# Kernel optimization log

Hardware: AMD Instinct MI355X
Metric: run time of the kernel (lower is better)

The kernel has to match this reference:

```python
import jax, jax.numpy as jnp
import numpy as np

N, K, C, S = 40000, 16, 128, 8  # points, neighbors, channels, share_planes
EPS = 1e-5


def _bn(x, g, b, m, v):
    # eval-mode BatchNorm1d over the channel (last) axis
    return (x - m) * (g * jax.lax.rsqrt(v + EPS)) + b


def _forward(xyz, feats, Wq, bq, Wk, bk, Wv, bv, Wp1, bp1, p_gamma, p_beta, p_mean, p_var,
             Wp2, bp2, w_gamma, w_beta, w_mean, w_var, Ww1, bw1, w1_gamma, w1_beta,
             w1_mean, w1_var, Ww2, bw2, nei_ind):
    x = feats[0]          # (N, C)
    pos = xyz[0]          # (N, 3)
    idx = nei_ind[0]      # (N, K)

    q = x @ Wq + bq                      # (N, C)
    kf = (x @ Wk + bk)[idx]              # (N, K, C) neighbor gather
    vf = (x @ Wv + bv)[idx]              # (N, K, C)

    d = pos[idx] - pos[:, None, :]       # (N, K, 3) relative positions
    # linear_p: Linear_BN(3,3) -> ReLU -> Linear(3, C)
    p = jax.nn.relu(_bn(d @ Wp1 + bp1, p_gamma, p_beta, p_mean, p_var)) @ Wp2 + bp2  # (N, K, C)

    # mid_planes == out_planes, so the view(...,1,mid).sum(2) is an identity reshape
    w = kf - q[:, None, :] + p           # (N, K, C)
    w = _bn(w, w_gamma, w_beta, w_mean, w_var)  # bn_w over channels
    # linear_w: ReLU -> Linear_BN(C, C//S) -> ReLU -> Linear(C//S, C//S)
    w = jax.nn.relu(_bn(jax.nn.relu(w) @ Ww1 + bw1, w1_gamma, w1_beta, w1_mean, w1_var)) @ Ww2 + bw2  # (N, K, C//S)
    w = jax.nn.softmax(w, axis=1)        # softmax over K neighbors

    # grouped-channel weighted sum over neighbors
    agg = ((vf + p).reshape(N, K, S, C // S) * w[:, :, None, :]).sum(axis=1).reshape(N, C)

    # shortcut is Identity (in_planes == out_planes); broadcast over batch dim like torch
    return jax.nn.leaky_relu(agg[None, :, :] + feats, negative_slope=0.1)  # (1, N, C)


def setup_inputs() -> dict:
    key = jax.random.key(0)
    ks = jax.random.split(key, 16)
    f32 = jnp.float32

    def w(k, shape, scale):
        return jax.random.normal(k, shape, dtype=f32) * scale

    return {
        "xyz": jax.random.uniform(ks[0], (1, N, 3), dtype=f32),
        "feats": jax.random.normal(ks[1], (1, N, C), dtype=f32),
        "nei_ind": jax.random.randint(ks[2], (1, N, K), 0, N, dtype=jnp.int32),
        "Wq": w(ks[3], (C, C), C ** -0.5), "bq": jnp.zeros((C,), f32),
        "Wk": w(ks[4], (C, C), C ** -0.5), "bk": jnp.zeros((C,), f32),
        "Wv": w(ks[5], (C, C), C ** -0.5), "bv": jnp.zeros((C,), f32),
        "Wp1": w(ks[6], (3, 3), 0.5), "bp1": jnp.zeros((3,), f32),
        "p_gamma": jnp.ones((3,), f32), "p_beta": jnp.zeros((3,), f32),
        "p_mean": w(ks[7], (3,), 0.1), "p_var": jnp.ones((3,), f32),
        "Wp2": w(ks[8], (3, C), 0.5), "bp2": jnp.zeros((C,), f32),
        "w_gamma": jnp.ones((C,), f32), "w_beta": jnp.zeros((C,), f32),
        "w_mean": w(ks[9], (C,), 0.1), "w_var": jnp.ones((C,), f32),
        "Ww1": w(ks[10], (C, C // S), C ** -0.5), "bw1": jnp.zeros((C // S,), f32),
        "w1_gamma": jnp.ones((C // S,), f32), "w1_beta": jnp.zeros((C // S,), f32),
        "w1_mean": w(ks[11], (C // S,), 0.1), "w1_var": jnp.ones((C // S,), f32),
        "Ww2": w(ks[12], (C // S, C // S), (C // S) ** -0.5), "bw2": jnp.zeros((C // S,), f32),
    }


def reference(xyz, feats, nei_ind, Wq, bq, Wk, bk, Wv, bv, Wp1, bp1, p_gamma, p_beta,
              p_mean, p_var, Wp2, bp2, w_gamma, w_beta, w_mean, w_var, Ww1, bw1,
              w1_gamma, w1_beta, w1_mean, w1_var, Ww2, bw2):
    return _forward(xyz, feats, Wq, bq, Wk, bk, Wv, bv, Wp1, bp1, p_gamma, p_beta,
                    p_mean, p_var, Wp2, bp2, w_gamma, w_beta, w_mean, w_var, Ww1, bw1,
                    w1_gamma, w1_beta, w1_mean, w1_var, Ww2, bw2, nei_ind)
```

## Files before the change

kernel.cpp:

```cpp
#include <hip/hip_runtime.h>
#include <stdint.h>

#define N_PTS 40000
#define KNBR  16
#define CH    128
#define EPSV  1e-5f

typedef __attribute__((ext_vector_type(4))) float f32x4;
typedef __attribute__((ext_vector_type(2))) float f32x2;
typedef __attribute__((ext_vector_type(8))) short bf16x8;

__device__ __forceinline__ float bf2f(ushort u) {
    union { uint32_t i; float f; } x; x.i = ((uint32_t)u) << 16; return x.f;
}
__device__ __forceinline__ float bflo(uint32_t u) {
    union { uint32_t i; float f; } x; x.i = u << 16; return x.f;
}
__device__ __forceinline__ float bfhi(uint32_t u) {
    union { uint32_t i; float f; } x; x.i = u & 0xffff0000u; return x.f;
}
__device__ __forceinline__ ushort f2bf(float f) {
    union { float f; uint32_t i; } x; x.f = f;
    uint32_t i = x.i;
    i += 0x7fffu + ((i >> 16) & 1u);
    return (ushort)(i >> 16);
}
__device__ __forceinline__ f32x2 unpk2(uint32_t u) {
    f32x2 r; r.x = bflo(u); r.y = bfhi(u); return r;
}
__device__ __forceinline__ f32x2 vmax2(f32x2 a, f32x2 b) {
#if __has_builtin(__builtin_elementwise_max)
    return __builtin_elementwise_max(a, b);
#else
    f32x2 r; r.x = fmaxf(a.x, b.x); r.y = fmaxf(a.y, b.y); return r;
#endif
}

__device__ __forceinline__ float rfl(float x) {
    union { float f; int i; } u; u.f = x;
    u.i = __builtin_amdgcn_readfirstlane(u.i);
    return u.f;
}

#if __has_builtin(__builtin_amdgcn_cvt_pk_bf16_f32)
typedef __bf16 bf16x2v __attribute__((ext_vector_type(2)));
__device__ __forceinline__ uint32_t pack2(float a, float b) {
    union { bf16x2v v; uint32_t u; } x;
    x.v = __builtin_amdgcn_cvt_pk_bf16_f32(a, b);
    return x.u;
}
#else
__device__ __forceinline__ uint32_t pack2(float a, float b) {
    return (uint32_t)f2bf(a) | ((uint32_t)f2bf(b) << 16);
}
#endif

template <bool BF> struct IO;
template <> struct IO<true> {
    static __device__ __forceinline__ float  ld (const void* p, int i) { return bf2f(((const ushort*)p)[i]); }
    static __device__ __forceinline__ float2 ld2(const void* p, int i) { const uint32_t u = ((const uint32_t*)p)[i]; return make_float2(bflo(u), bfhi(u)); }
    static __device__ __forceinline__ ushort ldbf(const void* p, int i) { return ((const ushort*)p)[i]; }
    static __device__ __forceinline__ void   st2(void* p, int i, float a, float b) { ((uint32_t*)p)[i] = pack2(a, b); }
};
template <> struct IO<false> {
    static __device__ __forceinline__ float  ld (const void* p, int i) { return ((const float*)p)[i]; }
    static __device__ __forceinline__ float2 ld2(const void* p, int i) { return ((const float2*)p)[i]; }
    static __device__ __forceinline__ ushort ldbf(const void* p, int i) { return f2bf(((const float*)p)[i]); }
    static __device__ __forceinline__ void   st2(void* p, int i, float a, float b) { ((float2*)p)[i] = make_float2(a, b); }
};

__device__ __forceinline__ bool detect_bf16(const void* w_var) {
    return (*(const uint32_t*)w_var & 0xffffu) != 0u;
}

template <bool BF>
__device__ void wtrans_body(const void* Wq, const void* Wk, const void* Wv,
                            ushort* wt)
{
    const int m    = blockIdx.x >> 4;
    const int part = blockIdx.x & 15;
    const void* W = (m == 0) ? Wq : (m == 1) ? Wk : Wv;
    const int base = part * 1024 + threadIdx.x * 4;
    #pragma unroll
    for (int e = 0; e < 4; ++e) {
        const int idx = base + e;
        const int k = idx >> 7;
        const int c = idx & 127;
        wt[m * 16384 + c * 128 + k] = IO<BF>::ldbf(W, idx);
    }
}

__global__ __launch_bounds__(256) void wtrans_kernel(
    const void* Wq, const void* Wk, const void* Wv, const void* w_var_probe,
    ushort* wt)
{
    if (detect_bf16(w_var_probe)) wtrans_body<true >(Wq, Wk, Wv, wt);
    else                          wtrans_body<false>(Wq, Wk, Wv, wt);
}

#define PROJ_BLOCKS 1250
template <bool BF>
__device__ void proj_body(
    const void* feats, const ushort* __restrict__ wt,
    const void* bq, const void* bk, const void* bv,
    uint32_t* qws, uint4* kvws,
    ushort* xs, uint32_t* qs_s, uint32_t* kv_s)
{
    const int tid  = threadIdx.x;
    const int l    = tid & 63;
    const int w    = tid >> 6;
    const int t    = l & 15;
    const int quad = l >> 4;
    const int cq   = w;

    const void* bsrc[3] = { bq, bk, bv };

    bf16x8 afrag[3][4];
    float  bias[3][4];
    #pragma unroll
    for (int m = 0; m < 3; ++m) {
        const ushort* wtm = wt + m * 16384 + (cq * 16 + t) * 128 + quad * 8;
        #pragma unroll
        for (int s = 0; s < 4; ++s)
            afrag[m][s] = *(const bf16x8*)(wtm + s * 32);
        #pragma unroll
        for (int r = 0; r < 4; ++r)
            bias[m][r] = IO<BF>::ld(bsrc[m], cq * 16 + quad * 4 + r);
    }

    #pragma unroll 1
    for (int n = 0; n < 2; ++n) {
        const int tt = blockIdx.x + PROJ_BLOCKS * n;
        const int p0 = tt * 16;

        {
            const int r   = tid >> 5;
            const int c32 = tid & 31;
            if (BF) {
                const ushort4 v = *(const ushort4*)((const ushort*)feats + (p0 + r) * CH + c32 * 4);
                *(ushort4*)&xs[r * 136 + c32 * 4] = v;
            } else {
                const float4 v = *(const float4*)((const float*)feats + (p0 + r) * CH + c32 * 4);
                ushort4 o;
                o.x = f2bf(v.x); o.y = f2bf(v.y); o.z = f2bf(v.z); o.w = f2bf(v.w);
                *(ushort4*)&xs[r * 136 + c32 * 4] = o;
            }
        }
        __syncthreads();

        bf16x8 bfr[4];
        #pragma unroll
        for (int s = 0; s < 4; ++s)
            bfr[s] = *(const bf16x8*)&xs[t * 136 + quad * 8 + s * 32];

        f32x4 acc[3];
        #pragma unroll
        for (int m = 0; m < 3; ++m) {
            acc[m] = f32x4{ bias[m][0], bias[m][1], bias[m][2], bias[m][3] };
            #pragma unroll
            for (int s = 0; s < 4; ++s)
                acc[m] = __builtin_amdgcn_mfma_f32_16x16x32_bf16(afrag[m][s], bfr[s], acc[m], 0, 0, 0);
        }

        const int m16 = cq * 4 + quad;
        uint2 qo;
        qo.x = pack2(acc[0][0], acc[0][1]);
        qo.y = pack2(acc[0][2], acc[0][3]);
        *(uint2*)&qs_s[t * 66 + m16 * 2] = qo;
        uint4 kv;
        kv.x = pack2(acc[1][0], acc[1][1]);
        kv.y = pack2(acc[2][0], acc[2][1]);
        kv.z = pack2(acc[1][2], acc[1][3]);
        kv.w = pack2(acc[2][2], acc[2][3]);
        *(uint4*)&kv_s[t * 132 + m16 * 4] = kv;
        __syncthreads();

        {
            const int r = tid >> 5;
            const int u = tid & 31;
            ((uint2*)qws)[(p0 + r) * 32 + u] = *(const uint2*)&qs_s[r * 66 + u * 2];
            kvws[(p0 + r) * 32 + u]          = *(const uint4*)&kv_s[r * 132 + u * 4];
        }
    }
}

__global__ __launch_bounds__(512) void proj_kernel(
    const void* feats, const ushort* __restrict__ wt,
    const void* bq, const void* bk, const void* bv, const void* w_var_probe,
    uint32_t* qws, uint4* kvws)
{
    __shared__ ushort   xs[16 * 136];
    __shared__ uint32_t qs_s[16 * 66];
    __shared__ uint32_t kv_s[16 * 132];
    if (detect_bf16(w_var_probe))
        proj_body<true >(feats, wt, bq, bk, bv, qws, kvws, xs, qs_s, kv_s);
    else
        proj_body<false>(feats, wt, bq, bk, bv, qws, kvws, xs, qs_s, kv_s);
}

template <bool BF>
__device__ void attn_body(
    const void* xyz, const void* feats, const int* __restrict__ nei,
    const uint32_t* __restrict__ qws, const uint2* __restrict__ kvws,
    const void* Wp1, const void* bp1, const void* p_gamma, const void* p_beta,
    const void* p_mean, const void* p_var, const void* Wp2, const void* bp2,
    const void* w_gamma, const void* w_beta, const void* w_mean, const void* w_var,
    const void* Ww1, const void* bw1, const void* w1_gamma, const void* w1_beta,
    const void* w1_mean, const void* w1_var, const void* Ww2, const void* bw2,
    void* out, ushort* wbuf, ushort* ubuf, float* wsm, float* hlds,
    int i0, int l)
{
    const int t = l & 15;
    const int quad = l >> 4;

    float A1[3][3], C1[3];
    #pragma unroll
    for (int b = 0; b < 3; ++b) {
        const float sb = IO<BF>::ld(p_gamma, b) * rsqrtf(IO<BF>::ld(p_var, b) + EPSV);
        C1[b] = rfl((IO<BF>::ld(bp1, b) - IO<BF>::ld(p_mean, b)) * sb + IO<BF>::ld(p_beta, b));
        #pragma unroll
        for (int a = 0; a < 3; ++a) A1[a][b] = rfl(IO<BF>::ld(Wp1, a * 3 + b) * sb);
    }

    const float2 vg = IO<BF>::ld2(w_gamma, l);
    const float2 vb = IO<BF>::ld2(w_beta, l);
    const float2 vm = IO<BF>::ld2(w_mean, l);
    const float2 vv = IO<BF>::ld2(w_var, l);
    f32x2 scwv, shwv;
    scwv.x = vg.x * rsqrtf(vv.x + EPSV);
    scwv.y = vg.y * rsqrtf(vv.y + EPSV);
    shwv.x = vb.x - vm.x * scwv.x;
    shwv.y = vb.y - vm.y * scwv.y;

    f32x2 wp2v[3];
    #pragma unroll
    for (int r = 0; r < 3; ++r) {
        const float2 u = IO<BF>::ld2(Wp2, r * 64 + l);
        wp2v[r].x = u.x; wp2v[r].y = u.y;
    }
    const float2 vbp2 = IO<BF>::ld2(bp2, l);
    f32x2 bp2v; bp2v.x = vbp2.x; bp2v.y = vbp2.y;

    bf16x8 bfrag1[4];
    #pragma unroll
    for (int s = 0; s < 4; ++s)
        #pragma unroll
        for (int kk = 0; kk < 8; ++kk) {
            const int k = s * 32 + quad * 8 + kk;
            bfrag1[s][kk] = (short)IO<BF>::ldbf(Ww1, k * 16 + t);
        }
    bf16x8 bfrag2;
    #pragma unroll
    for (int kk = 0; kk < 8; ++kk) {
        const int k = quad * 8 + kk;
        bfrag2[kk] = (quad < 2) ? (short)IO<BF>::ldbf(Ww2, k * 16 + t) : (short)0;
    }

    const float s1t  = IO<BF>::ld(w1_gamma, t) * rsqrtf(IO<BF>::ld(w1_var, t) + EPSV);
    const float sh1t = IO<BF>::ld(w1_beta, t) - IO<BF>::ld(w1_mean, t) * s1t;
    const float bw1t = IO<BF>::ld(bw1, t);
    const float bw2t = IO<BF>::ld(bw2, t);

    #pragma unroll 1
    for (int pp = 0; pp < 4; ++pp) {
        const int i = i0 + pp;

        const uint32_t uq = qws[i * 64 + l];
        const f32x2 qsv = shwv - unpk2(uq) * scwv;

        const float pix = IO<BF>::ld(xyz, i * 3 + 0);
        const float piy = IO<BF>::ld(xyz, i * 3 + 1);
        const float piz = IO<BF>::ld(xyz, i * 3 + 2);

        const int vnj = nei[i * KNBR + t];
        const float ndx = IO<BF>::ld(xyz, vnj * 3 + 0) - pix;
        const float ndy = IO<BF>::ld(xyz, vnj * 3 + 1) - piy;
        const float ndz = IO<BF>::ld(xyz, vnj * 3 + 2) - piz;
        const float hh0 = fmaxf(0.f, ndx * A1[0][0] + ndy * A1[1][0] + ndz * A1[2][0] + C1[0]);
        const float hh1 = fmaxf(0.f, ndx * A1[0][1] + ndy * A1[1][1] + ndz * A1[2][1] + C1[1]);
        const float hh2 = fmaxf(0.f, ndx * A1[0][2] + ndy * A1[1][2] + ndz * A1[2][2] + C1[2]);
        if (quad == 0)
            *(float4*)&hlds[t * 4] = make_float4(hh0, hh1, hh2, 0.f);

        int njs[KNBR];
        #pragma unroll
        for (int j = 0; j < KNBR; ++j) njs[j] = nei[i * KNBR + j];
        uint2 kv[KNBR];
        #pragma unroll
        for (int j = 0; j < KNBR; ++j) kv[j] = kvws[njs[j] * 64 + l];

        uint32_t vpk[KNBR];
        #pragma unroll
        for (int j = 0; j < KNBR; ++j) {
            const float4 h = *(const float4*)&hlds[j * 4];
            const f32x2 pv = h.x * wp2v[0] + h.y * wp2v[1] + h.z * wp2v[2] + bp2v;
            vpk[j] = kv[j].y;
            const f32x2 wv = vmax2((unpk2(kv[j].x) + pv) * scwv + qsv,
                                   f32x2{0.f, 0.f});
            ((uint32_t*)wbuf)[j * 68 + l] = pack2(wv.x, wv.y);
        }

        f32x4 acc1 = { bw1t, bw1t, bw1t, bw1t };
        const ushort* arow = &wbuf[t * 136 + quad * 8];
        #pragma unroll
        for (int s = 0; s < 4; ++s) {
            const bf16x8 afrag = *(const bf16x8*)(arow + s * 32);
            acc1 = __builtin_amdgcn_mfma_f32_16x16x32_bf16(afrag, bfrag1[s], acc1, 0, 0, 0);
        }
        #pragma unroll
        for (int r = 0; r < 4; ++r) {
            const float u = fmaxf(0.f, acc1[r] * s1t + sh1t);
            ubuf[(quad * 4 + r) * 24 + t] = f2bf(u);
        }

        f32x4 acc2 = { bw2t, bw2t, bw2t, bw2t };
        bf16x8 afrag2;
        if (quad < 2) {
            afrag2 = *(const bf16x8*)(&ubuf[t * 24 + quad * 8]);
        } else {
            #pragma unroll
            for (int kk = 0; kk < 8; ++kk) afrag2[kk] = 0;
        }
        acc2 = __builtin_amdgcn_mfma_f32_16x16x32_bf16(afrag2, bfrag2, acc2, 0, 0, 0);

        float z0 = acc2[0], z1 = acc2[1], z2 = acc2[2], z3 = acc2[3];
        float mx = fmaxf(fmaxf(z0, z1), fmaxf(z2, z3));
        mx = fmaxf(mx, __shfl_xor(mx, 16));
        mx = fmaxf(mx, __shfl_xor(mx, 32));
        const float e0 = __expf(z0 - mx), e1 = __expf(z1 - mx);
        const float e2 = __expf(z2 - mx), e3 = __expf(z3 - mx);
        float ssum = e0 + e1 + e2 + e3;
        ssum += __shfl_xor(ssum, 16);
        ssum += __shfl_xor(ssum, 32);
        const float inv = 1.0f / ssum;
        wsm[(quad * 4 + 0) * 17 + t] = e0 * inv;
        wsm[(quad * 4 + 1) * 17 + t] = e1 * inv;
        wsm[(quad * 4 + 2) * 17 + t] = e2 * inv;
        wsm[(quad * 4 + 3) * 17 + t] = e3 * inv;

        const int t0 = (2 * l) & 15;
        f32x2 aggv = { 0.f, 0.f };
        #pragma unroll
        for (int j = 0; j < KNBR; ++j) {
            f32x2 wp;
            wp.x = wsm[j * 17 + t0];
            wp.y = wsm[j * 17 + t0 + 1];
            const float4 h = *(const float4*)&hlds[j * 4];
            const f32x2 pv = h.x * wp2v[0] + h.y * wp2v[1] + h.z * wp2v[2] + bp2v;
            aggv += (unpk2(vpk[j]) + pv) * wp;
        }
        const float2 xf = IO<BF>::ld2(feats, i * 64 + l);
        f32x2 ov; ov.x = aggv.x + xf.x; ov.y = aggv.y + xf.y;
        ov = vmax2(ov, 0.1f * ov);
        IO<BF>::st2(out, i * 64 + l, ov.x, ov.y);
    }
}

__global__ __launch_bounds__(256) void attn_kernel(
    const void* xyz, const void* feats, const int* __restrict__ nei,
    const uint32_t* __restrict__ qws, const uint2* __restrict__ kvws,
    const void* Wp1, const void* bp1, const void* p_gamma, const void* p_beta,
    const void* p_mean, const void* p_var, const void* Wp2, const void* bp2,
    const void* w_gamma, const void* w_beta, const void* w_mean, const void* w_var,
    const void* Ww1, const void* bw1, const void* w1_gamma, const void* w1_beta,
    const void* w1_mean, const void* w1_var, const void* Ww2, const void* bw2,
    void* out)
{
    __shared__ ushort wbuf[4][16 * 136];
    __shared__ float  hlds[4][16 * 4];

    const int wave = threadIdx.x >> 6;
    const int l    = threadIdx.x & 63;
    const int i0   = blockIdx.x * 16 + wave * 4;

    ushort* wb  = wbuf[wave];
    ushort* ub  = wb;
    float*  wsm = (float*)((char*)wb + 1024);

    if (detect_bf16(w_var))
        attn_body<true >(xyz, feats, nei, qws, kvws, Wp1, bp1, p_gamma, p_beta,
                         p_mean, p_var, Wp2, bp2, w_gamma, w_beta, w_mean, w_var,
                         Ww1, bw1, w1_gamma, w1_beta, w1_mean, w1_var, Ww2, bw2,
                         out, wb, ub, wsm, hlds[wave], i0, l);
    else
        attn_body<false>(xyz, feats, nei, qws, kvws, Wp1, bp1, p_gamma, p_beta,
                         p_mean, p_var, Wp2, bp2, w_gamma, w_beta, w_mean, w_var,
                         Ww1, bw1, w1_gamma, w1_beta, w1_mean, w1_var, Ww2, bw2,
                         out, wb, ub, wsm, hlds[wave], i0, l);
}

extern "C" void kernel_launch(void* const* d_in, const int* in_sizes, int n_in,
                              void* d_out, int out_size, void* d_ws, size_t ws_size,
                              hipStream_t stream) {
    const void* xyz     = d_in[0];
    const void* feats   = d_in[1];
    const int*  nei     = (const int*)d_in[2];
    const void* Wq      = d_in[3];
    const void* bq      = d_in[4];
    const void* Wk      = d_in[5];
    const void* bk      = d_in[6];
    const void* Wv      = d_in[7];
    const void* bv      = d_in[8];
    const void* Wp1     = d_in[9];
    const void* bp1     = d_in[10];
    const void* p_gamma = d_in[11];
    const void* p_beta  = d_in[12];
    const void* p_mean  = d_in[13];
    const void* p_var   = d_in[14];
    const void* Wp2     = d_in[15];
    const void* bp2     = d_in[16];
    const void* w_gamma = d_in[17];
    const void* w_beta  = d_in[18];
    const void* w_mean  = d_in[19];
    const void* w_var   = d_in[20];
    const void* Ww1     = d_in[21];
    const void* bw1     = d_in[22];
    const void* w1_gamma= d_in[23];
    const void* w1_beta = d_in[24];
    const void* w1_mean = d_in[25];
    const void* w1_var  = d_in[26];
    const void* Ww2     = d_in[27];
    const void* bw2     = d_in[28];

    uint32_t* qws  = (uint32_t*)d_ws;
    uint4*    kvws = (uint4*)(qws + (size_t)N_PTS * 64);

    const size_t base = (size_t)N_PTS * 64 * 4 + (size_t)N_PTS * 32 * 16;
    ushort* wt = (ws_size >= base + 3 * 16384 * sizeof(ushort))
               ? (ushort*)((char*)d_ws + base)
               : (ushort*)d_out;

    wtrans_kernel<<<48, 256, 0, stream>>>(Wq, Wk, Wv, w_var, wt);
    proj_kernel<<<PROJ_BLOCKS, 512, 0, stream>>>(feats, wt, bq, bk, bv, w_var,
                                                 qws, kvws);
    attn_kernel<<<N_PTS / 16, 256, 0, stream>>>(xyz, feats, nei, qws, (const uint2*)kvws,
                                          Wp1, bp1, p_gamma, p_beta, p_mean, p_var,
                                          Wp2, bp2, w_gamma, w_beta, w_mean, w_var,
                                          Ww1, bw1, w1_gamma, w1_beta, w1_mean, w1_var,
                                          Ww2, bw2, d_out);
}
```

Measured before the change: 214.9 us.

## Process more points per wave, cache v+p in registers, separate LDS buffers

Doubles the points handled per wave, so each block covers 32 points and the per-wave setup of weight fragments and BN constants is amortised over more points, at the cost of half as many blocks. The v+p values are now computed once in the first neighbor loop and kept as float pairs in registers, replacing the recomputation of the position encoding in the aggregation loop but raising register pressure. The ubuf and wsm scratch arrays get their own LDS regions instead of aliasing wbuf, the softmax weights use stride 18 so they can be read as 8-byte vectors, and the readfirstlane hints on the scalar constants are dropped.

```diff
diff --git a/kernel.cpp b/kernel.cpp
--- a/kernel.cpp
+++ b/kernel.cpp
@@ -5,6 +5,9 @@
 #define KNBR  16
 #define CH    128
 #define EPSV  1e-5f
+
+#define PTS_PER_WAVE 8
+#define PTS_PER_BLOCK (PTS_PER_WAVE * 4)
 
 typedef __attribute__((ext_vector_type(4))) float f32x4;
 typedef __attribute__((ext_vector_type(2))) float f32x2;
@@ -34,12 +37,6 @@
 #else
     f32x2 r; r.x = fmaxf(a.x, b.x); r.y = fmaxf(a.y, b.y); return r;
 #endif
-}
-
-__device__ __forceinline__ float rfl(float x) {
-    union { float f; int i; } u; u.f = x;
-    u.i = __builtin_amdgcn_readfirstlane(u.i);
-    return u.f;
 }
 
 #if __has_builtin(__builtin_amdgcn_cvt_pk_bf16_f32)
@@ -217,9 +214,9 @@
     #pragma unroll
     for (int b = 0; b < 3; ++b) {
         const float sb = IO<BF>::ld(p_gamma, b) * rsqrtf(IO<BF>::ld(p_var, b) + EPSV);
-        C1[b] = rfl((IO<BF>::ld(bp1, b) - IO<BF>::ld(p_mean, b)) * sb + IO<BF>::ld(p_beta, b));
-        #pragma unroll
-        for (int a = 0; a < 3; ++a) A1[a][b] = rfl(IO<BF>::ld(Wp1, a * 3 + b) * sb);
+        C1[b] = (IO<BF>::ld(bp1, b) - IO<BF>::ld(p_mean, b)) * sb + IO<BF>::ld(p_beta, b);
+        #pragma unroll
+        for (int a = 0; a < 3; ++a) A1[a][b] = IO<BF>::ld(Wp1, a * 3 + b) * sb;
     }
 
     const float2 vg = IO<BF>::ld2(w_gamma, l);
@@ -262,7 +259,7 @@
     const float bw2t = IO<BF>::ld(bw2, t);
 
     #pragma unroll 1
-    for (int pp = 0; pp < 4; ++pp) {
+    for (int pp = 0; pp < PTS_PER_WAVE; ++pp) {
         const int i = i0 + pp;
 
         const uint32_t uq = qws[i * 64 + l];
@@ -289,12 +286,15 @@
         #pragma unroll
         for (int j = 0; j < KNBR; ++j) kv[j] = kvws[njs[j] * 64 + l];
 
-        uint32_t vpk[KNBR];
+        f32x2 vfp[KNBR];
         #pragma unroll
         for (int j = 0; j < KNBR; ++j) {
             const float4 h = *(const float4*)&hlds[j * 4];
-            const f32x2 pv = h.x * wp2v[0] + h.y * wp2v[1] + h.z * wp2v[2] + bp2v;
-            vpk[j] = kv[j].y;
+            f32x2 pv = bp2v;
+            pv += h.x * wp2v[0];
+            pv += h.y * wp2v[1];
+            pv += h.z * wp2v[2];
+            vfp[j] = unpk2(kv[j].y) + pv;
             const f32x2 wv = vmax2((unpk2(kv[j].x) + pv) * scwv + qsv,
                                    f32x2{0.f, 0.f});
             ((uint32_t*)wbuf)[j * 68 + l] = pack2(wv.x, wv.y);
@@ -333,21 +333,17 @@
         ssum += __shfl_xor(ssum, 16);
         ssum += __shfl_xor(ssum, 32);
         const float inv = 1.0f / ssum;
-        wsm[(quad * 4 + 0) * 17 + t] = e0 * inv;
-        wsm[(quad * 4 + 1) * 17 + t] = e1 * inv;
-        wsm[(quad * 4 + 2) * 17 + t] = e2 * inv;
-        wsm[(quad * 4 + 3) * 17 + t] = e3 * inv;
+        wsm[(quad * 4 + 0) * 18 + t] = e0 * inv;
+        wsm[(quad * 4 + 1) * 18 + t] = e1 * inv;
+        wsm[(quad * 4 + 2) * 18 + t] = e2 * inv;
+        wsm[(quad * 4 + 3) * 18 + t] = e3 * inv;
 
         const int t0 = (2 * l) & 15;
         f32x2 aggv = { 0.f, 0.f };
         #pragma unroll
         for (int j = 0; j < KNBR; ++j) {
-            f32x2 wp;
-            wp.x = wsm[j * 17 + t0];
-            wp.y = wsm[j * 17 + t0 + 1];
-            const float4 h = *(const float4*)&hlds[j * 4];
-            const f32x2 pv = h.x * wp2v[0] + h.y * wp2v[1] + h.z * wp2v[2] + bp2v;
-            aggv += (unpk2(vpk[j]) + pv) * wp;
+            const f32x2 wp = *(const f32x2*)&wsm[j * 18 + t0];
+            aggv += vfp[j] * wp;
         }
         const float2 xf = IO<BF>::ld2(feats, i * 64 + l);
         f32x2 ov; ov.x = aggv.x + xf.x; ov.y = aggv.y + xf.y;
@@ -367,26 +363,24 @@
     void* out)
 {
     __shared__ ushort wbuf[4][16 * 136];
+    __shared__ ushort ubuf[4][16 * 24];
+    __shared__ float  wsm [4][16 * 18];
     __shared__ float  hlds[4][16 * 4];
 
     const int wave = threadIdx.x >> 6;
     const int l    = threadIdx.x & 63;
-    const int i0   = blockIdx.x * 16 + wave * 4;
-
-    ushort* wb  = wbuf[wave];
-    ushort* ub  = wb;
-    float*  wsm = (float*)((char*)wb + 1024);
+    const int i0   = blockIdx.x * PTS_PER_BLOCK + wave * PTS_PER_WAVE;
 
     if (detect_bf16(w_var))
         attn_body<true >(xyz, feats, nei, qws, kvws, Wp1, bp1, p_gamma, p_beta,
                          p_mean, p_var, Wp2, bp2, w_gamma, w_beta, w_mean, w_var,
                          Ww1, bw1, w1_gamma, w1_beta, w1_mean, w1_var, Ww2, bw2,
-                         out, wb, ub, wsm, hlds[wave], i0, l);
+                         out, wbuf[wave], ubuf[wave], wsm[wave], hlds[wave], i0, l);
     else
         attn_body<false>(xyz, feats, nei, qws, kvws, Wp1, bp1, p_gamma, p_beta,
                          p_mean, p_var, Wp2, bp2, w_gamma, w_beta, w_mean, w_var,
                          Ww1, bw1, w1_gamma, w1_beta, w1_mean, w1_var, Ww2, bw2,
-                         out, wb, ub, wsm, hlds[wave], i0, l);
+                         out, wbuf[wave], ubuf[wave], wsm[wave], hlds[wave], i0, l);
 }
 
 extern "C" void kernel_launch(void* const* d_in, const int* in_sizes, int n_in,
@@ -433,7 +427,8 @@
     wtrans_kernel<<<48, 256, 0, stream>>>(Wq, Wk, Wv, w_var, wt);
     proj_kernel<<<PROJ_BLOCKS, 512, 0, stream>>>(feats, wt, bq, bk, bv, w_var,
                                                  qws, kvws);
-    attn_kernel<<<N_PTS / 16, 256, 0, stream>>>(xyz, feats, nei, qws, (const uint2*)kvws,
+    attn_kernel<<<N_PTS / PTS_PER_BLOCK, 256, 0, stream>>>(
+                                          xyz, feats, nei, qws, (const uint2*)kvws,
                                           Wp1, bp1, p_gamma, p_beta, p_mean, p_var,
                                           Wp2, bp2, w_gamma, w_beta, w_mean, w_var,
                                           Ww1, bw1, w1_gamma, w1_beta, w1_mean, w1_var,
```

After: 208.6 us. 1.03x faster.
